# Kernel optimization log

Measured on AMD Instinct MI355X. Metric: run time of the kernel, lower is better.

## Reference

```python
import jax, jax.numpy as jnp
import numpy as np

B, S, D = 2, 2048, 1024
H, DK, DV = 16, 64, 64

def setup_inputs() -> dict:
    key = jax.random.key(0)
    ks = jax.random.split(key, 5)
    scale = 1.0 / np.sqrt(D)  # xavier-ish
    return {
        "Q": jax.random.normal(ks[0], (B, S, D), dtype=jnp.float32),
        "attn_mask": jax.random.uniform(ks[1], (B, S), dtype=jnp.float32),
        "W_Q": jax.random.normal(ks[2], (H * DK, D), dtype=jnp.float32) * scale,
        "b_Q": jnp.zeros((H * DK,), dtype=jnp.float32),
        "W_K": jax.random.normal(ks[3], (H * DK, D), dtype=jnp.float32) * scale,
        "b_K": jnp.zeros((H * DK,), dtype=jnp.float32),
        "W_V": jax.random.normal(ks[4], (H * DV, D), dtype=jnp.float32) * scale,
        "b_V": jnp.zeros((H * DV,), dtype=jnp.float32),
    }

def reference(Q, attn_mask, W_Q, b_Q, W_K, b_K, W_V, b_V):
    b, s, _ = Q.shape
    # projections -> [B, H, S, d]
    q = (Q @ W_Q.T + b_Q).reshape(b, s, H, DK).transpose(0, 2, 1, 3)
    k = (Q @ W_K.T + b_K).reshape(b, s, H, DK).transpose(0, 2, 1, 3)
    v = (Q @ W_V.T + b_V).reshape(b, s, H, DV).transpose(0, 2, 1, 3)
    # exp-based attention (NOT stable softmax), multiplicative mask
    scores = jnp.einsum('bhqd,bhkd->bhqk', q, k) / np.sqrt(DK)
    scores = jnp.exp(scores)
    # mask [B, S_key] broadcast over heads and queries -> [B, 1, 1, S]
    scores = scores * attn_mask[:, None, None, :]
    attn = scores / (jnp.sum(scores, axis=-1, keepdims=True) + 1e-8)
    context = jnp.einsum('bhqk,bhkd->bhqd', attn, v)
    # [B, H, S, DV] -> [B, S, H*DV]
    return context.transpose(0, 2, 1, 3).reshape(b, s, H * DV)
```

## Files before the change

### kernel.cpp

```cpp
#include <hip/hip_runtime.h>
#include <hip/hip_bf16.h>
#include <math.h>

#define BATCH  2
#define S_LEN  2048
#define DMODEL 1024
#define NH     16
#define DHEAD  64

typedef __attribute__((ext_vector_type(8))) short bf16x8;
typedef __attribute__((ext_vector_type(4))) float f32x4;

#define MFMA16(a,b,c) __builtin_amdgcn_mfma_f32_16x16x32_bf16((a),(b),(c),0,0,0)

#define QSCALE 0.18033688011110793f
#define EXP2F(x) __builtin_amdgcn_exp2f(x)

__device__ __forceinline__ unsigned int pkbf(float a, float b) {
    __hip_bfloat162 h = __float22bfloat162_rn(make_float2(a, b));
    union { __hip_bfloat162 h; unsigned int u; } v; v.h = h; return v.u;
}
__device__ __forceinline__ void gl2lds16(const void* g, void* l) {
    __builtin_amdgcn_global_load_lds(
        (const __attribute__((address_space(1))) void*)(g),
        (__attribute__((address_space(3))) void*)(l), 16, 0, 0);
}

__global__ __launch_bounds__(256) void cvt_all(
    const float* __restrict__ Q,  const float* __restrict__ WQ,
    const float* __restrict__ WK, const float* __restrict__ WV,
    const float* __restrict__ msk,
    unsigned short* __restrict__ Qbf, unsigned short* __restrict__ Wbf,
    unsigned short* __restrict__ mbf)
{
    int i = blockIdx.x * blockDim.x + threadIdx.x;
    const float* src;
    unsigned short* dst;
    int off;
    if (i < 524288) {
        src = Q; dst = Qbf; off = i;
    } else if (i < 917504) {
        int j = i - 524288;
        int which = j >> 17;
        src = (which == 0) ? WQ : ((which == 1) ? WK : WV);
        dst = Wbf + ((size_t)which << 20);
        off = j & 131071;
    } else {
        int j = i - 917504;
        if (j >= 512) return;
        src = msk; dst = mbf; off = j;
    }
    float4 a = ((const float4*)src)[2*off];
    float4 b = ((const float4*)src)[2*off + 1];
    uint4 o;
    o.x = pkbf(a.x, a.y); o.y = pkbf(a.z, a.w);
    o.z = pkbf(b.x, b.y); o.w = pkbf(b.z, b.w);
    ((uint4*)dst)[off] = o;
}

__global__ __launch_bounds__(256) void proj_mfma(
    const unsigned short* __restrict__ Abf,
    const unsigned short* __restrict__ Wbf,
    const float* __restrict__ bQ, const float* __restrict__ bK,
    const float* __restrict__ bV, const float* __restrict__ mask,
    unsigned short* __restrict__ qw, unsigned short* __restrict__ kw,
    unsigned short* __restrict__ vt)
{
    __shared__ union {
        struct { unsigned short At[128*32]; unsigned short Bt[128*32]; } s;
        unsigned short Ct[128*132];
    } sm;

    const int tid  = threadIdx.x;
    const int lane = tid & 63;
    const int wv   = tid >> 6;
    const int wm   = (wv >> 1) * 64;
    const int wn   = (wv & 1) * 64;
    const int q15  = lane & 15;
    const int quad = lane >> 4;
    const int z    = blockIdx.z;
    const int n0   = blockIdx.x * 128;
    const int m0   = blockIdx.y * 128;

    const unsigned short* Wz = Wbf + (size_t)z * DMODEL * DMODEL;
    const float* bias = (z == 0) ? bQ : ((z == 1) ? bK : bV);

    f32x4 zero4 = {0.f, 0.f, 0.f, 0.f};
    f32x4 acc[4][4];
    #pragma unroll
    for (int i = 0; i < 4; ++i)
        #pragma unroll
        for (int j = 0; j < 4; ++j) acc[i][j] = zero4;

    for (int k0 = 0; k0 < DMODEL; k0 += 32) {
        __syncthreads();
        #pragma unroll
        for (int c = 0; c < 2; ++c) {
            int o   = tid * 16 + c * 4096;
            int row = o >> 6;
            int cb  = o & 63;
            gl2lds16(Abf + (size_t)(m0 + row) * DMODEL + k0 + (cb >> 1),
                     (char*)sm.s.At + o);
            gl2lds16(Wz  + (size_t)(n0 + row) * DMODEL + k0 + (cb >> 1),
                     (char*)sm.s.Bt + o);
        }
        __syncthreads();

        bf16x8 af[4], bf[4];
        #pragma unroll
        for (int i = 0; i < 4; ++i)
            af[i] = *(const bf16x8*)(sm.s.At + (wm + i*16 + q15) * 32 + quad * 8);
        #pragma unroll
        for (int j = 0; j < 4; ++j)
            bf[j] = *(const bf16x8*)(sm.s.Bt + (wn + j*16 + q15) * 32 + quad * 8);

        if (z < 2) {
            #pragma unroll
            for (int i = 0; i < 4; ++i)
                #pragma unroll
                for (int j = 0; j < 4; ++j)
                    acc[i][j] = MFMA16(bf[j], af[i], acc[i][j]);
        } else {
            #pragma unroll
            for (int i = 0; i < 4; ++i)
                #pragma unroll
                for (int j = 0; j < 4; ++j)
                    acc[i][j] = MFMA16(af[i], bf[j], acc[i][j]);
        }
    }

    __syncthreads();

    if (z < 2) {
        const float qs = (z == 0) ? QSCALE : 1.0f;
        #pragma unroll
        for (int i = 0; i < 4; ++i) {
            int ml = wm + i*16 + q15;
            #pragma unroll
            for (int j = 0; j < 4; ++j) {
                int nl = wn + j*16 + quad*4;
                float4 b4 = *(const float4*)(bias + n0 + nl);
                f32x4 v = acc[i][j];
                uint2 u;
                u.x = pkbf((v.x + b4.x)*qs, (v.y + b4.y)*qs);
                u.y = pkbf((v.z + b4.z)*qs, (v.w + b4.w)*qs);
                *(uint2*)&sm.Ct[ml*132 + nl] = u;
            }
        }
    } else {
        #pragma unroll
        for (int i = 0; i < 4; ++i) {
            int ml = wm + i*16 + quad*4;
            int sg = m0 + ml;
            int b2 = sg >> 11, s0g = sg & 2047;
            float4 mk4 = *(const float4*)(mask + (size_t)b2*S_LEN + s0g);
            #pragma unroll
            for (int j = 0; j < 4; ++j) {
                int nl = wn + j*16 + q15;
                float bv = bias[n0 + nl];
                f32x4 v = acc[i][j];
                uint2 u;
                u.x = pkbf((v.x + bv)*mk4.x, (v.y + bv)*mk4.y);
                u.y = pkbf((v.z + bv)*mk4.z, (v.w + bv)*mk4.w);
                *(uint2*)&sm.Ct[nl*132 + ml] = u;
            }
        }
    }
    __syncthreads();

    {
        int row  = tid >> 1;
        int half = (tid & 1) * 64;
        const uint4* src = (const uint4*)&sm.Ct[row*132 + half];
        unsigned short* dst;
        if (z < 2) {
            unsigned short* outp = (z == 0) ? qw : kw;
            int mg = m0 + row;  int b2 = mg >> 11, s = mg & 2047;
            int n  = n0 + half; int hh = n >> 6;
            dst = outp + (((size_t)b2*NH + hh)*S_LEN + s)*DHEAD;
        } else {
            int n  = n0 + row;  int hh = n >> 6, dv = n & 63;
            int b2 = m0 >> 11, s0 = m0 & 2047;
            dst = vt + (((size_t)b2*NH + hh)*DHEAD + dv)*S_LEN + s0 + half;
        }
        #pragma unroll
        for (int c = 0; c < 8; ++c) ((uint4*)dst)[c] = src[c];
    }
}

__global__ __launch_bounds__(256, 2) void attn_mfma(
    const unsigned short* __restrict__ qw, const unsigned short* __restrict__ kw,
    const unsigned short* __restrict__ vt, const unsigned short* __restrict__ mbf,
    float* __restrict__ out)
{
    __shared__ __align__(16) unsigned short Ks[2][64][72];
    __shared__ __align__(16) unsigned short Vs[2][64][72];
    __shared__ __align__(16) unsigned short Ms[2][72];

    const int tid  = threadIdx.x;
    const int lane = tid & 63;
    const int wv   = tid >> 6;
    const int q15  = lane & 15;
    const int quad = lane >> 4;
    const int q0   = blockIdx.x * 128;
    const int h    = blockIdx.y;
    const int b    = blockIdx.z;

    const size_t headoff = ((size_t)b * NH + h) * S_LEN * DHEAD;
    const unsigned short* qb = qw + headoff;
    const unsigned short* kb = kw + headoff;
    const unsigned short* vb = vt + headoff;
    const unsigned short* mb = mbf + (size_t)b * S_LEN;

    bf16x8 qf[2][2];
    #pragma unroll
    for (int qi = 0; qi < 2; ++qi) {
        const unsigned short* qr = qb + (size_t)(q0 + wv*32 + qi*16 + q15)*DHEAD;
        qf[qi][0] = *(const bf16x8*)(qr + quad*8);
        qf[qi][1] = *(const bf16x8*)(qr + 32 + quad*8);
    }

    const int srow = tid >> 3;
    const int scol = (tid & 7) * 8;
    const int prow = ((srow >> 2) & 1) * 16 + ((srow >> 3) & 3) * 4 + (srow & 3);

    f32x4 zero4 = {0.f, 0.f, 0.f, 0.f};
    f32x4 oacc[2][4];
    f32x4 dacc[2];
    #pragma unroll
    for (int qi = 0; qi < 2; ++qi) {
        dacc[qi] = zero4;
        #pragma unroll
        for (int nj = 0; nj < 4; ++nj) oacc[qi][nj] = zero4;
    }

    uint4 kr0, kr1, vr0, vr1, mr = {0,0,0,0};
    kr0 = *(const uint4*)(kb + (size_t)(srow)     *DHEAD + scol);
    kr1 = *(const uint4*)(kb + (size_t)(srow + 32)*DHEAD + scol);
    vr0 = *(const uint4*)(vb + (size_t)(srow)     *S_LEN + scol);
    vr1 = *(const uint4*)(vb + (size_t)(srow + 32)*S_LEN + scol);
    if (tid < 8) mr = *(const uint4*)(mb + tid*8);

    for (int t = 0; t < 32; ++t) {
        const int buf = t & 1;
        const int k0  = t * 64;
        *(uint4*)&Ks[buf][prow][scol]      = kr0;
        *(uint4*)&Ks[buf][prow + 32][scol] = kr1;
        *(uint4*)&Vs[buf][srow][scol]      = vr0;
        *(uint4*)&Vs[buf][srow + 32][scol] = vr1;
        if (tid < 8) *(uint4*)&Ms[buf][tid*8] = mr;
        const int kn = (t < 31) ? k0 + 64 : 0;
        kr0 = *(const uint4*)(kb + (size_t)(kn + srow)     *DHEAD + scol);
        kr1 = *(const uint4*)(kb + (size_t)(kn + srow + 32)*DHEAD + scol);
        vr0 = *(const uint4*)(vb + (size_t)(srow)     *S_LEN + kn + scol);
        vr1 = *(const uint4*)(vb + (size_t)(srow + 32)*S_LEN + kn + scol);
        if (tid < 8) mr = *(const uint4*)(mb + kn + tid*8);
        __syncthreads();

        f32x4 s[2][4];
        #pragma unroll
        for (int ks = 0; ks < 4; ++ks) {
            bf16x8 kf0 = *(const bf16x8*)&Ks[buf][ks*16 + q15][quad*8];
            bf16x8 kf1 = *(const bf16x8*)&Ks[buf][ks*16 + q15][32 + quad*8];
            #pragma unroll
            for (int qi = 0; qi < 2; ++qi) {
                f32x4 a = MFMA16(kf0, qf[qi][0], zero4);
                s[qi][ks] = MFMA16(kf1, qf[qi][1], a);
            }
        }
        bf16x8 pf[2][2];
        #pragma unroll
        for (int qi = 0; qi < 2; ++qi) {
            uint4 u0, u1;
            u0.x = pkbf(EXP2F(s[qi][0][0]), EXP2F(s[qi][0][1]));
            u0.y = pkbf(EXP2F(s[qi][0][2]), EXP2F(s[qi][0][3]));
            u0.z = pkbf(EXP2F(s[qi][1][0]), EXP2F(s[qi][1][1]));
            u0.w = pkbf(EXP2F(s[qi][1][2]), EXP2F(s[qi][1][3]));
            u1.x = pkbf(EXP2F(s[qi][2][0]), EXP2F(s[qi][2][1]));
            u1.y = pkbf(EXP2F(s[qi][2][2]), EXP2F(s[qi][2][3]));
            u1.z = pkbf(EXP2F(s[qi][3][0]), EXP2F(s[qi][3][1]));
            u1.w = pkbf(EXP2F(s[qi][3][2]), EXP2F(s[qi][3][3]));
            union { uint4 u; bf16x8 h; } c0, c1;
            c0.u = u0; c1.u = u1;
            pf[qi][0] = c0.h;
            pf[qi][1] = c1.h;
        }
        bf16x8 mf0 = *(const bf16x8*)&Ms[buf][quad*8];
        bf16x8 mf1 = *(const bf16x8*)&Ms[buf][32 + quad*8];
        #pragma unroll
        for (int qi = 0; qi < 2; ++qi) {
            dacc[qi] = MFMA16(pf[qi][0], mf0, dacc[qi]);
            dacc[qi] = MFMA16(pf[qi][1], mf1, dacc[qi]);
        }
        #pragma unroll
        for (int nj = 0; nj < 4; ++nj) {
            bf16x8 vf0 = *(const bf16x8*)&Vs[buf][nj*16 + q15][quad*8];
            bf16x8 vf1 = *(const bf16x8*)&Vs[buf][nj*16 + q15][32 + quad*8];
            #pragma unroll
            for (int qi = 0; qi < 2; ++qi) {
                oacc[qi][nj] = MFMA16(pf[qi][0], vf0, oacc[qi][nj]);
                oacc[qi][nj] = MFMA16(pf[qi][1], vf1, oacc[qi][nj]);
            }
        }
    }

    #pragma unroll
    for (int qi = 0; qi < 2; ++qi)
        #pragma unroll
        for (int r = 0; r < 4; ++r) {
            float inv = 1.0f / (dacc[qi][r] + 1e-8f);
            size_t row = ((size_t)b*S_LEN + q0 + wv*32 + qi*16 + quad*4 + r)*DMODEL
                       + h*DHEAD;
            #pragma unroll
            for (int nj = 0; nj < 4; ++nj)
                out[row + nj*16 + q15] = oacc[qi][nj][r] * inv;
        }
}

extern "C" void kernel_launch(void* const* d_in, const int* in_sizes, int n_in,
                              void* d_out, int out_size, void* d_ws, size_t ws_size,
                              hipStream_t stream) {
    const float* Q    = (const float*)d_in[0];
    const float* msk  = (const float*)d_in[1];
    const float* W_Q  = (const float*)d_in[2];
    const float* b_Q  = (const float*)d_in[3];
    const float* W_K  = (const float*)d_in[4];
    const float* b_K  = (const float*)d_in[5];
    const float* W_V  = (const float*)d_in[6];
    const float* b_V  = (const float*)d_in[7];
    float* out = (float*)d_out;

    unsigned short* wsu = (unsigned short*)d_ws;
    unsigned short* Qbf = wsu;
    unsigned short* Wbf = Qbf + (size_t)4096*1024;
    unsigned short* qwb = Wbf + (size_t)3*1024*1024;
    unsigned short* kwb = qwb + (size_t)4*1024*1024;
    unsigned short* vtb = kwb + (size_t)4*1024*1024;
    unsigned short* mbf = vtb + (size_t)4*1024*1024;

    cvt_all<<<3586, 256, 0, stream>>>(Q, W_Q, W_K, W_V, msk, Qbf, Wbf, mbf);

    proj_mfma<<<dim3(8, 32, 3), 256, 0, stream>>>(
        Qbf, Wbf, b_Q, b_K, b_V, msk, qwb, kwb, vtb);

    attn_mfma<<<dim3(S_LEN/128, NH, BATCH), 256, 0, stream>>>(
        qwb, kwb, vtb, mbf, out);
}
```

Before: 184.0 us.

## Double-buffer projection GEMM with K=64 tiles, swizzled LDS, and block remap

The projection GEMM now stages 64-wide K tiles into two LDS buffers, so the next tile's global-to-LDS load is issued while MFMAs run on the current one. This halves the number of loop iterations and cuts the barriers per iteration from two to one. LDS rows are XOR-swizzled to avoid bank conflicts on the wider rows, and block indices are remapped so consecutive blocks share A/W tiles, aiming for better L2 reuse. The cost is more LDS (64KB), which may lower occupancy.

```diff
diff --git a/kernel.cpp b/kernel.cpp
--- a/kernel.cpp
+++ b/kernel.cpp
@@ -67,7 +67,7 @@
     unsigned short* __restrict__ vt)
 {
     __shared__ union {
-        struct { unsigned short At[128*32]; unsigned short Bt[128*32]; } s;
+        struct { unsigned short At[2][128*64]; unsigned short Bt[2][128*64]; } s;
         unsigned short Ct[128*132];
     } sm;
 
@@ -78,9 +78,13 @@
     const int wn   = (wv & 1) * 64;
     const int q15  = lane & 15;
     const int quad = lane >> 4;
-    const int z    = blockIdx.z;
-    const int n0   = blockIdx.x * 128;
-    const int m0   = blockIdx.y * 128;
+
+    const int f  = blockIdx.x + (blockIdx.y << 3) + (blockIdx.z << 8);
+    const int l  = (f & 7) * 96 + (f >> 3);
+    const int z  = l >> 8;
+    const int lr = l & 255;
+    const int n0 = (lr & 7) * 128;
+    const int m0 = (lr >> 3) * 128;
 
     const unsigned short* Wz = Wbf + (size_t)z * DMODEL * DMODEL;
     const float* bias = (z == 0) ? bQ : ((z == 1) ? bK : bV);
@@ -92,44 +96,58 @@
         #pragma unroll
         for (int j = 0; j < 4; ++j) acc[i][j] = zero4;
 
-    for (int k0 = 0; k0 < DMODEL; k0 += 32) {
+    #define STAGE_PROJ(BUF, K0)                                                \
+        _Pragma("unroll")                                                      \
+        for (int c = 0; c < 4; ++c) {                                          \
+            int o   = tid * 16 + c * 4096;                                     \
+            int row = o >> 7;                                                  \
+            int lb  = (o & 127) ^ ((row & 7) << 4);                            \
+            gl2lds16(Abf + (size_t)(m0 + row) * DMODEL + (K0) + (lb >> 1),     \
+                     (char*)sm.s.At[BUF] + o);                                 \
+            gl2lds16(Wz  + (size_t)(n0 + row) * DMODEL + (K0) + (lb >> 1),     \
+                     (char*)sm.s.Bt[BUF] + o);                                 \
+        }
+
+    STAGE_PROJ(0, 0)
+    __syncthreads();
+
+    const int sw = (q15 & 7) << 4;
+
+    for (int t = 0; t < 16; ++t) {
+        const int buf = t & 1;
+        if (t < 15) { STAGE_PROJ(buf ^ 1, (t + 1) * 64) }
+
+        bf16x8 af[4][2], bfr[4][2];
+        #pragma unroll
+        for (int i = 0; i < 4; ++i) {
+            const char* pa = (const char*)sm.s.At[buf] + (wm + i*16 + q15) * 128;
+            const char* pb = (const char*)sm.s.Bt[buf] + (wn + i*16 + q15) * 128;
+            af[i][0]  = *(const bf16x8*)(pa + (( 0 + quad*16) ^ sw));
+            af[i][1]  = *(const bf16x8*)(pa + ((64 + quad*16) ^ sw));
+            bfr[i][0] = *(const bf16x8*)(pb + (( 0 + quad*16) ^ sw));
+            bfr[i][1] = *(const bf16x8*)(pb + ((64 + quad*16) ^ sw));
+        }
+
+        if (z < 2) {
+            #pragma unroll
+            for (int ks = 0; ks < 2; ++ks)
+                #pragma unroll
+                for (int i = 0; i < 4; ++i)
+                    #pragma unroll
+                    for (int j = 0; j < 4; ++j)
+                        acc[i][j] = MFMA16(bfr[j][ks], af[i][ks], acc[i][j]);
+        } else {
+            #pragma unroll
+            for (int ks = 0; ks < 2; ++ks)
+                #pragma unroll
+                for (int i = 0; i < 4; ++i)
+                    #pragma unroll
+                    for (int j = 0; j < 4; ++j)
+                        acc[i][j] = MFMA16(af[i][ks], bfr[j][ks], acc[i][j]);
+        }
         __syncthreads();
-        #pragma unroll
-        for (int c = 0; c < 2; ++c) {
-            int o   = tid * 16 + c * 4096;
-            int row = o >> 6;
-            int cb  = o & 63;
-            gl2lds16(Abf + (size_t)(m0 + row) * DMODEL + k0 + (cb >> 1),
-                     (char*)sm.s.At + o);
-            gl2lds16(Wz  + (size_t)(n0 + row) * DMODEL + k0 + (cb >> 1),
-                     (char*)sm.s.Bt + o);
-        }
-        __syncthreads();
-
-        bf16x8 af[4], bf[4];
-        #pragma unroll
-        for (int i = 0; i < 4; ++i)
-            af[i] = *(const bf16x8*)(sm.s.At + (wm + i*16 + q15) * 32 + quad * 8);
-        #pragma unroll
-        for (int j = 0; j < 4; ++j)
-            bf[j] = *(const bf16x8*)(sm.s.Bt + (wn + j*16 + q15) * 32 + quad * 8);
-
-        if (z < 2) {
-            #pragma unroll
-            for (int i = 0; i < 4; ++i)
-                #pragma unroll
-                for (int j = 0; j < 4; ++j)
-                    acc[i][j] = MFMA16(bf[j], af[i], acc[i][j]);
-        } else {
-            #pragma unroll
-            for (int i = 0; i < 4; ++i)
-                #pragma unroll
-                for (int j = 0; j < 4; ++j)
-                    acc[i][j] = MFMA16(af[i], bf[j], acc[i][j]);
-        }
-    }
-
-    __syncthreads();
+    }
+    #undef STAGE_PROJ
 
     if (z < 2) {
         const float qs = (z == 0) ? QSCALE : 1.0f;
```

Measured after the change: 171.4 us. -6.8%, faster.
